# Optimization experiments

Measured on AMD Instinct MI355X. Metric: run time of the kernel, lower is better.

Reference implementation:

```python
import jax, jax.numpy as jnp
import numpy as np


def setup_inputs() -> dict:
    key = jax.random.key(0)
    k1, k2, k3, k4, k5, k6 = jax.random.split(key, 6)
    bs, sl, max_nw, dim_vtw, dim_hidden = 32, 1024, 16, 64, 128
    xw = jax.random.normal(k1, (bs, sl, max_nw, dim_vtw), dtype=jnp.float32)
    # xn: [bs, sl, ns+1]; only last column (word length, in [1, max_nw]) is used
    xn = jax.random.randint(k2, (bs, sl, 4), 1, max_nw + 1)
    s = 1.0 / np.sqrt(dim_hidden)
    W_ih = jax.random.uniform(k3, (4 * dim_hidden, dim_vtw), minval=-s, maxval=s, dtype=jnp.float32)
    W_hh = jax.random.uniform(k4, (4 * dim_hidden, dim_hidden), minval=-s, maxval=s, dtype=jnp.float32)
    b_ih = jax.random.uniform(k5, (4 * dim_hidden,), minval=-s, maxval=s, dtype=jnp.float32)
    b_hh = jax.random.uniform(k6, (4 * dim_hidden,), minval=-s, maxval=s, dtype=jnp.float32)
    return {"xw": xw, "xn": xn, "W_ih": W_ih, "W_hh": W_hh, "b_ih": b_ih, "b_hh": b_hh}


def reference(xw, xn, W_ih, W_hh, b_ih, b_hh):
    # Vectorized equivalent of the original per-group loop: run the LSTM over
    # the full max_nw timesteps for every (b, s) position (LSTM is causal, so
    # the hidden state after nw steps equals running only the first nw steps),
    # then gather h at t = length-1 per position.
    bs, sl, T, D = xw.shape
    H = W_hh.shape[1]
    N = bs * sl
    x = xw.reshape(N, T, D)
    lengths = xn[:, :, -1].reshape(N)
    # Precompute input contributions to all 4 gates: [T, N, 4H]
    x_gates = jnp.einsum('ntd,gd->tng', x, W_ih) + (b_ih + b_hh)

    def step(carry, xg):
        h, c = carry
        gates = xg + h @ W_hh.T  # [N, 4H]
        i, f, g, o = jnp.split(gates, 4, axis=-1)
        i = jax.nn.sigmoid(i)
        f = jax.nn.sigmoid(f)
        g = jnp.tanh(g)
        o = jax.nn.sigmoid(o)
        c = f * c + i * g
        h = o * jnp.tanh(c)
        return (h, c), h

    init = (jnp.zeros((N, H), xw.dtype), jnp.zeros((N, H), xw.dtype))
    _, hs = jax.lax.scan(step, init, x_gates)  # hs: [T, N, H]
    hs = jnp.swapaxes(hs, 0, 1)  # [N, T, H]
    idx = jnp.clip(lengths - 1, 0, T - 1)
    h_final = jnp.take_along_axis(hs, idx[:, None, None], axis=1)[:, 0]  # [N, H]
    return h_final.reshape(bs, sl, H)
```

## Files before the change

kernel.cpp:

```cpp
#include <hip/hip_runtime.h>
#include <math.h>

#define T_STEPS 16
#define DIM_X 64
#define DIM_H 128
#define DIM_K 192
#define NPACK 512
#define MSEQ 64
#define NTHREADS 512
#define LDK 200

typedef __attribute__((ext_vector_type(8))) short bf16x8;
typedef __attribute__((ext_vector_type(4))) float f32x4;

__device__ __forceinline__ float fsigmoid(float x) {
    return 1.0f / (1.0f + __expf(-x));
}
__device__ __forceinline__ float ftanh_(float x) {
    float a = fabsf(x);
    float e = __expf(2.0f * a);
    float r = 1.0f - 2.0f / (e + 1.0f);
    return copysignf(r, x);
}
__device__ __forceinline__ unsigned short bf16_rn(float x) {
    unsigned int b = __float_as_uint(x);
    b += 0x7FFFu + ((b >> 16) & 1u);
    return (unsigned short)(b >> 16);
}
__device__ __forceinline__ float bf16_to_f(unsigned short u) {
    return __uint_as_float(((unsigned int)u) << 16);
}

__global__ void pack_weights(const float* __restrict__ W_ih, const float* __restrict__ W_hh,
                             const float* __restrict__ b_ih, const float* __restrict__ b_hh,
                             unsigned short* __restrict__ Whi, unsigned short* __restrict__ Wlo,
                             float* __restrict__ bsum) {
    int i = blockIdx.x * blockDim.x + threadIdx.x;
    if (i >= NPACK * DIM_K) return;
    int p = i / DIM_K, k = i % DIM_K;
    int g = (p >> 4) & 3;
    int unit = ((p >> 6) << 4) + (p & 15);
    int r = g * DIM_H + unit;
    float v = (k < DIM_X) ? W_ih[r * DIM_X + k] : W_hh[r * DIM_H + (k - DIM_X)];
    unsigned short hi = bf16_rn(v);
    Whi[i] = hi;
    Wlo[i] = bf16_rn(v - bf16_to_f(hi));
    if (k == 0) bsum[p] = b_ih[r] + b_hh[r];
}

__global__ void bin_seqs(const int* __restrict__ xn, int N, int* __restrict__ list) {
    __shared__ int hist[T_STEPS], offs[T_STEPS], cur[T_STEPS];
    int tid = threadIdx.x;
    if (tid < T_STEPS) hist[tid] = 0;
    __syncthreads();
    for (int i = tid; i < N; i += blockDim.x) {
        int len = xn[i * 4 + 3];
        len = min(max(len, 1), T_STEPS);
        atomicAdd(&hist[len - 1], 1);
    }
    __syncthreads();
    if (tid == 0) {
        int acc = 0;
        for (int b = T_STEPS - 1; b >= 0; --b) { offs[b] = acc; acc += hist[b]; }
    }
    __syncthreads();
    if (tid < T_STEPS) cur[tid] = offs[tid];
    __syncthreads();
    for (int i = tid; i < N; i += blockDim.x) {
        int len = xn[i * 4 + 3];
        len = min(max(len, 1), T_STEPS);
        int pos = atomicAdd(&cur[len - 1], 1);
        list[pos] = i;
    }
}

__global__ __launch_bounds__(NTHREADS)
void lstm_main(const float* __restrict__ xw, const int* __restrict__ xn,
               const unsigned short* __restrict__ Whi, const unsigned short* __restrict__ Wlo,
               const float* __restrict__ bsum, const int* __restrict__ list,
               int N, float* __restrict__ out)
{
    __shared__ unsigned short xh_hi[MSEQ][LDK];
    __shared__ unsigned short xh_lo[MSEQ][LDK];
    __shared__ int s_seq[MSEQ];
    __shared__ int s_len[MSEQ];
    __shared__ int s_maxlen;

    const int tid = threadIdx.x;
    const int wv = tid >> 6;
    const int lane = tid & 63;
    const int lr = lane & 15;
    const int lh = lane >> 4;
    const int unit = (wv << 4) + lr;

    if (tid == 0) s_maxlen = 0;
    __syncthreads();
    if (tid < MSEQ) {
        int idx = blockIdx.x * MSEQ + tid;
        int seq = (idx < N) ? list[idx] : -1;
        s_seq[tid] = seq;
        int len = 0;
        if (seq >= 0) { len = xn[seq * 4 + 3]; len = min(max(len, 1), T_STEPS); }
        s_len[tid] = len;
        atomicMax(&s_maxlen, len);
    }
#pragma unroll
    for (int m = 0; m < 4; ++m)
#pragma unroll
        for (int j = 0; j < 4; ++j) {
            int s = (m << 4) + (lh << 2) + j;
            xh_hi[s][DIM_X + unit] = 0;
            xh_lo[s][DIM_X + unit] = 0;
        }
    __syncthreads();
    const int maxlen = s_maxlen;

    float bias[4];
#pragma unroll
    for (int g = 0; g < 4; ++g) bias[g] = bsum[(wv << 6) + (g << 4) + lr];

    int lenv[4][4];
#pragma unroll
    for (int m = 0; m < 4; ++m)
#pragma unroll
        for (int j = 0; j < 4; ++j) lenv[m][j] = s_len[(m << 4) + (lh << 2) + j];

    float c[4][4];
#pragma unroll
    for (int m = 0; m < 4; ++m)
#pragma unroll
        for (int j = 0; j < 4; ++j) c[m][j] = 0.0f;

    const int xsl = tid >> 3;
    const int xko = (tid & 7) << 3;
    const long xseq = (long)max(s_seq[xsl], 0);

    {
        const float* xp = xw + ((size_t)xseq * T_STEPS + 0) * DIM_X + xko;
        float4 a = *(const float4*)xp;
        float4 b = *(const float4*)(xp + 4);
        float xv[8] = {a.x, a.y, a.z, a.w, b.x, b.y, b.z, b.w};
        bf16x8 hv, lv;
#pragma unroll
        for (int e = 0; e < 8; ++e) {
            unsigned short h = bf16_rn(xv[e]);
            hv[e] = (short)h;
            lv[e] = (short)bf16_rn(xv[e] - bf16_to_f(h));
        }
        *(bf16x8*)&xh_hi[xsl][xko] = hv;
        *(bf16x8*)&xh_lo[xsl][xko] = lv;
    }

    const unsigned short* __restrict__ wbase_h = Whi + (size_t)(wv << 6) * DIM_K + (lh << 3);
    const unsigned short* __restrict__ wbase_l = Wlo + (size_t)(wv << 6) * DIM_K + (lh << 3);

    for (int t = 0; t < maxlen; ++t) {
        __syncthreads();

        f32x4 acc[4][4];
#pragma unroll
        for (int m = 0; m < 4; ++m)
#pragma unroll
            for (int g = 0; g < 4; ++g)
                acc[m][g] = (f32x4){bias[g], bias[g], bias[g], bias[g]};

        for (int kc = 0; kc < 6; ++kc) {
            const int kb = kc << 5;
            bf16x8 ahi[4], alo[4];
#pragma unroll
            for (int m = 0; m < 4; ++m) {
                ahi[m] = *(const bf16x8*)&xh_hi[(m << 4) + lr][kb + (lh << 3)];
                alo[m] = *(const bf16x8*)&xh_lo[(m << 4) + lr][kb + (lh << 3)];
            }
            bf16x8 bhi[4], blo[4];
#pragma unroll
            for (int g = 0; g < 4; ++g) {
                const size_t off = (size_t)((g << 4) + lr) * DIM_K + kb;
                bhi[g] = *(const bf16x8*)(wbase_h + off);
                blo[g] = *(const bf16x8*)(wbase_l + off);
            }
#pragma unroll
            for (int m = 0; m < 4; ++m)
#pragma unroll
                for (int g = 0; g < 4; ++g) {
                    acc[m][g] = __builtin_amdgcn_mfma_f32_16x16x32_bf16(ahi[m], bhi[g], acc[m][g], 0, 0, 0);
                    acc[m][g] = __builtin_amdgcn_mfma_f32_16x16x32_bf16(alo[m], bhi[g], acc[m][g], 0, 0, 0);
                    acc[m][g] = __builtin_amdgcn_mfma_f32_16x16x32_bf16(ahi[m], blo[g], acc[m][g], 0, 0, 0);
                }
        }

        const bool do_x = (t + 1 < maxlen);
        float4 xa, xb;
        if (do_x) {
            const float* xp = xw + ((size_t)xseq * T_STEPS + (t + 1)) * DIM_X + xko;
            xa = *(const float4*)xp;
            xb = *(const float4*)(xp + 4);
        }

        __syncthreads();

        if (do_x) {
            float xv[8] = {xa.x, xa.y, xa.z, xa.w, xb.x, xb.y, xb.z, xb.w};
            bf16x8 hv, lv;
#pragma unroll
            for (int e = 0; e < 8; ++e) {
                unsigned short h = bf16_rn(xv[e]);
                hv[e] = (short)h;
                lv[e] = (short)bf16_rn(xv[e] - bf16_to_f(h));
            }
            *(bf16x8*)&xh_hi[xsl][xko] = hv;
            *(bf16x8*)&xh_lo[xsl][xko] = lv;
        }

#pragma unroll
        for (int m = 0; m < 4; ++m)
#pragma unroll
            for (int j = 0; j < 4; ++j) {
                float iv = fsigmoid(acc[m][0][j]);
                float fv = fsigmoid(acc[m][1][j]);
                float gv = ftanh_(acc[m][2][j]);
                float ov = fsigmoid(acc[m][3][j]);
                float cv = fv * c[m][j] + iv * gv;
                c[m][j] = cv;
                float hv = ov * ftanh_(cv);
                int s = (m << 4) + (lh << 2) + j;
                unsigned short hh = bf16_rn(hv);
                xh_hi[s][DIM_X + unit] = hh;
                xh_lo[s][DIM_X + unit] = bf16_rn(hv - bf16_to_f(hh));
                if (t == lenv[m][j] - 1) {
                    int gs = s_seq[s];
                    if (gs >= 0) out[(size_t)gs * DIM_H + unit] = hv;
                }
            }
    }
}

extern "C" void kernel_launch(void* const* d_in, const int* in_sizes, int n_in,
                              void* d_out, int out_size, void* d_ws, size_t ws_size,
                              hipStream_t stream) {
    const float* xw   = (const float*)d_in[0];
    const int*   xn   = (const int*)d_in[1];
    const float* W_ih = (const float*)d_in[2];
    const float* W_hh = (const float*)d_in[3];
    const float* b_ih = (const float*)d_in[4];
    const float* b_hh = (const float*)d_in[5];
    float* out = (float*)d_out;

    const int N = in_sizes[0] / (T_STEPS * DIM_X);

    char* ws = (char*)d_ws;
    unsigned short* Whi = (unsigned short*)ws;
    unsigned short* Wlo = (unsigned short*)(ws + 196608);
    float*          bsum = (float*)(ws + 393216);
    int*            list = (int*)(ws + 395264);

    pack_weights<<<(NPACK * DIM_K + 255) / 256, 256, 0, stream>>>(W_ih, W_hh, b_ih, b_hh, Whi, Wlo, bsum);
    bin_seqs<<<1, 1024, 0, stream>>>(xn, N, list);

    const int nblocks = (N + MSEQ - 1) / MSEQ;
    lstm_main<<<nblocks, NTHREADS, 0, stream>>>(xw, xn, Whi, Wlo, bsum, list, N, out);
}
```

Baseline: 505.1 us.

## Use persistent blocks with atomic chunk queue and fuse prep kernels

Merges weight packing and length binning into one prep kernel, which also resets a work counter. The LSTM kernel becomes persistent: at most 256 blocks repeatedly grab 64-sequence chunks via an atomic counter. Because the list is sorted longest-first, the chunk max length is read from its first entry. Input loads and output stores use nontemporal hints. This aims to balance work across CUs and cut launch overhead, at the cost of less latency hiding from co-resident blocks and a shared-memory reuse race risk.

```diff
diff --git a/kernel.cpp b/kernel.cpp
--- a/kernel.cpp
+++ b/kernel.cpp
@@ -9,6 +9,9 @@
 #define MSEQ 64
 #define NTHREADS 512
 #define LDK 200
+#define PREP_THREADS 256
+#define PACK_ITEMS (NPACK * DIM_K)
+#define PACK_BLOCKS (PACK_ITEMS / PREP_THREADS)
 
 typedef __attribute__((ext_vector_type(8))) short bf16x8;
 typedef __attribute__((ext_vector_type(4))) float f32x4;
@@ -31,29 +34,32 @@
     return __uint_as_float(((unsigned int)u) << 16);
 }
 
-__global__ void pack_weights(const float* __restrict__ W_ih, const float* __restrict__ W_hh,
-                             const float* __restrict__ b_ih, const float* __restrict__ b_hh,
-                             unsigned short* __restrict__ Whi, unsigned short* __restrict__ Wlo,
-                             float* __restrict__ bsum) {
-    int i = blockIdx.x * blockDim.x + threadIdx.x;
-    if (i >= NPACK * DIM_K) return;
-    int p = i / DIM_K, k = i % DIM_K;
-    int g = (p >> 4) & 3;
-    int unit = ((p >> 6) << 4) + (p & 15);
-    int r = g * DIM_H + unit;
-    float v = (k < DIM_X) ? W_ih[r * DIM_X + k] : W_hh[r * DIM_H + (k - DIM_X)];
-    unsigned short hi = bf16_rn(v);
-    Whi[i] = hi;
-    Wlo[i] = bf16_rn(v - bf16_to_f(hi));
-    if (k == 0) bsum[p] = b_ih[r] + b_hh[r];
-}
-
-__global__ void bin_seqs(const int* __restrict__ xn, int N, int* __restrict__ list) {
+__global__ __launch_bounds__(PREP_THREADS)
+void prep(const float* __restrict__ W_ih, const float* __restrict__ W_hh,
+          const float* __restrict__ b_ih, const float* __restrict__ b_hh,
+          const int* __restrict__ xn, int N,
+          unsigned short* __restrict__ Whi, unsigned short* __restrict__ Wlo,
+          float* __restrict__ bsum, int* __restrict__ list, int* __restrict__ ctr) {
+    const int b = blockIdx.x;
+    const int tid = threadIdx.x;
+    if (b < PACK_BLOCKS) {
+        int i = b * PREP_THREADS + tid;
+        int p = i / DIM_K, k = i % DIM_K;
+        int g = (p >> 4) & 3;
+        int unit = ((p >> 6) << 4) + (p & 15);
+        int r = g * DIM_H + unit;
+        float v = (k < DIM_X) ? W_ih[r * DIM_X + k] : W_hh[r * DIM_H + (k - DIM_X)];
+        unsigned short hi = bf16_rn(v);
+        Whi[i] = hi;
+        Wlo[i] = bf16_rn(v - bf16_to_f(hi));
+        if (k == 0) bsum[p] = b_ih[r] + b_hh[r];
+        return;
+    }
     __shared__ int hist[T_STEPS], offs[T_STEPS], cur[T_STEPS];
-    int tid = threadIdx.x;
     if (tid < T_STEPS) hist[tid] = 0;
-    __syncthreads();
-    for (int i = tid; i < N; i += blockDim.x) {
+    if (tid == 0) *ctr = 0;
+    __syncthreads();
+    for (int i = tid; i < N; i += PREP_THREADS) {
         int len = xn[i * 4 + 3];
         len = min(max(len, 1), T_STEPS);
         atomicAdd(&hist[len - 1], 1);
@@ -61,12 +67,12 @@
     __syncthreads();
     if (tid == 0) {
         int acc = 0;
-        for (int b = T_STEPS - 1; b >= 0; --b) { offs[b] = acc; acc += hist[b]; }
+        for (int bb = T_STEPS - 1; bb >= 0; --bb) { offs[bb] = acc; acc += hist[bb]; }
     }
     __syncthreads();
     if (tid < T_STEPS) cur[tid] = offs[tid];
     __syncthreads();
-    for (int i = tid; i < N; i += blockDim.x) {
+    for (int i = tid; i < N; i += PREP_THREADS) {
         int len = xn[i * 4 + 3];
         len = min(max(len, 1), T_STEPS);
         int pos = atomicAdd(&cur[len - 1], 1);
@@ -78,13 +84,13 @@
 void lstm_main(const float* __restrict__ xw, const int* __restrict__ xn,
                const unsigned short* __restrict__ Whi, const unsigned short* __restrict__ Wlo,
                const float* __restrict__ bsum, const int* __restrict__ list,
-               int N, float* __restrict__ out)
+               int N, int* __restrict__ ctr, float* __restrict__ out)
 {
     __shared__ unsigned short xh_hi[MSEQ][LDK];
     __shared__ unsigned short xh_lo[MSEQ][LDK];
     __shared__ int s_seq[MSEQ];
     __shared__ int s_len[MSEQ];
-    __shared__ int s_maxlen;
+    __shared__ int s_chunk;
 
     const int tid = threadIdx.x;
     const int wv = tid >> 6;
@@ -92,115 +98,61 @@
     const int lr = lane & 15;
     const int lh = lane >> 4;
     const int unit = (wv << 4) + lr;
-
-    if (tid == 0) s_maxlen = 0;
-    __syncthreads();
-    if (tid < MSEQ) {
-        int idx = blockIdx.x * MSEQ + tid;
-        int seq = (idx < N) ? list[idx] : -1;
-        s_seq[tid] = seq;
-        int len = 0;
-        if (seq >= 0) { len = xn[seq * 4 + 3]; len = min(max(len, 1), T_STEPS); }
-        s_len[tid] = len;
-        atomicMax(&s_maxlen, len);
-    }
-#pragma unroll
-    for (int m = 0; m < 4; ++m)
-#pragma unroll
-        for (int j = 0; j < 4; ++j) {
-            int s = (m << 4) + (lh << 2) + j;
-            xh_hi[s][DIM_X + unit] = 0;
-            xh_lo[s][DIM_X + unit] = 0;
-        }
-    __syncthreads();
-    const int maxlen = s_maxlen;
+    const int nchunks = (N + MSEQ - 1) / MSEQ;
 
     float bias[4];
 #pragma unroll
     for (int g = 0; g < 4; ++g) bias[g] = bsum[(wv << 6) + (g << 4) + lr];
-
-    int lenv[4][4];
-#pragma unroll
-    for (int m = 0; m < 4; ++m)
-#pragma unroll
-        for (int j = 0; j < 4; ++j) lenv[m][j] = s_len[(m << 4) + (lh << 2) + j];
-
-    float c[4][4];
-#pragma unroll
-    for (int m = 0; m < 4; ++m)
-#pragma unroll
-        for (int j = 0; j < 4; ++j) c[m][j] = 0.0f;
+    const unsigned short* __restrict__ wbase_h = Whi + (size_t)(wv << 6) * DIM_K + (lh << 3);
+    const unsigned short* __restrict__ wbase_l = Wlo + (size_t)(wv << 6) * DIM_K + (lh << 3);
 
     const int xsl = tid >> 3;
     const int xko = (tid & 7) << 3;
-    const long xseq = (long)max(s_seq[xsl], 0);
-
-    {
-        const float* xp = xw + ((size_t)xseq * T_STEPS + 0) * DIM_X + xko;
-        float4 a = *(const float4*)xp;
-        float4 b = *(const float4*)(xp + 4);
-        float xv[8] = {a.x, a.y, a.z, a.w, b.x, b.y, b.z, b.w};
-        bf16x8 hv, lv;
-#pragma unroll
-        for (int e = 0; e < 8; ++e) {
-            unsigned short h = bf16_rn(xv[e]);
-            hv[e] = (short)h;
-            lv[e] = (short)bf16_rn(xv[e] - bf16_to_f(h));
+
+    while (true) {
+        if (tid == 0) s_chunk = atomicAdd(ctr, 1);
+        __syncthreads();
+        const int chunk = s_chunk;
+        if (chunk >= nchunks) break;
+
+        if (tid < MSEQ) {
+            int idx = chunk * MSEQ + tid;
+            int seq = (idx < N) ? list[idx] : -1;
+            s_seq[tid] = seq;
+            int len = 0;
+            if (seq >= 0) { len = xn[seq * 4 + 3]; len = min(max(len, 1), T_STEPS); }
+            s_len[tid] = len;
         }
-        *(bf16x8*)&xh_hi[xsl][xko] = hv;
-        *(bf16x8*)&xh_lo[xsl][xko] = lv;
-    }
-
-    const unsigned short* __restrict__ wbase_h = Whi + (size_t)(wv << 6) * DIM_K + (lh << 3);
-    const unsigned short* __restrict__ wbase_l = Wlo + (size_t)(wv << 6) * DIM_K + (lh << 3);
-
-    for (int t = 0; t < maxlen; ++t) {
+#pragma unroll
+        for (int m = 0; m < 4; ++m)
+#pragma unroll
+            for (int j = 0; j < 4; ++j) {
+                int s = (m << 4) + (lh << 2) + j;
+                xh_hi[s][DIM_X + unit] = 0;
+                xh_lo[s][DIM_X + unit] = 0;
+            }
         __syncthreads();
 
-        f32x4 acc[4][4];
+        const int maxlen = s_len[0];
+        int lenv[4][4];
 #pragma unroll
         for (int m = 0; m < 4; ++m)
 #pragma unroll
-            for (int g = 0; g < 4; ++g)
-                acc[m][g] = (f32x4){bias[g], bias[g], bias[g], bias[g]};
-
-        for (int kc = 0; kc < 6; ++kc) {
-            const int kb = kc << 5;
-            bf16x8 ahi[4], alo[4];
-#pragma unroll
-            for (int m = 0; m < 4; ++m) {
-                ahi[m] = *(const bf16x8*)&xh_hi[(m << 4) + lr][kb + (lh << 3)];
-                alo[m] = *(const bf16x8*)&xh_lo[(m << 4) + lr][kb + (lh << 3)];
-            }
-            bf16x8 bhi[4], blo[4];
-#pragma unroll
-            for (int g = 0; g < 4; ++g) {
-                const size_t off = (size_t)((g << 4) + lr) * DIM_K + kb;
-                bhi[g] = *(const bf16x8*)(wbase_h + off);
-                blo[g] = *(const bf16x8*)(wbase_l + off);
-            }
-#pragma unroll
-            for (int m = 0; m < 4; ++m)
-#pragma unroll
-                for (int g = 0; g < 4; ++g) {
-                    acc[m][g] = __builtin_amdgcn_mfma_f32_16x16x32_bf16(ahi[m], bhi[g], acc[m][g], 0, 0, 0);
-                    acc[m][g] = __builtin_amdgcn_mfma_f32_16x16x32_bf16(alo[m], bhi[g], acc[m][g], 0, 0, 0);
-                    acc[m][g] = __builtin_amdgcn_mfma_f32_16x16x32_bf16(ahi[m], blo[g], acc[m][g], 0, 0, 0);
-                }
-        }
-
-        const bool do_x = (t + 1 < maxlen);
-        float4 xa, xb;
-        if (do_x) {
-            const float* xp = xw + ((size_t)xseq * T_STEPS + (t + 1)) * DIM_X + xko;
-            xa = *(const float4*)xp;
-            xb = *(const float4*)(xp + 4);
-        }
-
-        __syncthreads();
-
-        if (do_x) {
-            float xv[8] = {xa.x, xa.y, xa.z, xa.w, xb.x, xb.y, xb.z, xb.w};
+            for (int j = 0; j < 4; ++j) lenv[m][j] = s_len[(m << 4) + (lh << 2) + j];
+
+        float c[4][4];
+#pragma unroll
+        for (int m = 0; m < 4; ++m)
+#pragma unroll
+            for (int j = 0; j < 4; ++j) c[m][j] = 0.0f;
+
+        const long xseq = (long)max(s_seq[xsl], 0);
+
+        {
+            const float* xp = xw + ((size_t)xseq * T_STEPS + 0) * DIM_X + xko;
+            f32x4 a = __builtin_nontemporal_load((const f32x4*)xp);
+            f32x4 bq = __builtin_nontemporal_load((const f32x4*)(xp + 4));
+            float xv[8] = {a[0], a[1], a[2], a[3], bq[0], bq[1], bq[2], bq[3]};
             bf16x8 hv, lv;
 #pragma unroll
             for (int e = 0; e < 8; ++e) {
@@ -212,26 +164,86 @@
             *(bf16x8*)&xh_lo[xsl][xko] = lv;
         }
 
-#pragma unroll
-        for (int m = 0; m < 4; ++m)
-#pragma unroll
-            for (int j = 0; j < 4; ++j) {
-                float iv = fsigmoid(acc[m][0][j]);
-                float fv = fsigmoid(acc[m][1][j]);
-                float gv = ftanh_(acc[m][2][j]);
-                float ov = fsigmoid(acc[m][3][j]);
-                float cv = fv * c[m][j] + iv * gv;
-                c[m][j] = cv;
-                float hv = ov * ftanh_(cv);
-                int s = (m << 4) + (lh << 2) + j;
-                unsigned short hh = bf16_rn(hv);
-                xh_hi[s][DIM_X + unit] = hh;
-                xh_lo[s][DIM_X + unit] = bf16_rn(hv - bf16_to_f(hh));
-                if (t == lenv[m][j] - 1) {
-                    int gs = s_seq[s];
-                    if (gs >= 0) out[(size_t)gs * DIM_H + unit] = hv;
-                }
-            }
+        for (int t = 0; t < maxlen; ++t) {
+            __syncthreads();
+
+            f32x4 acc[4][4];
+#pragma unroll
+            for (int m = 0; m < 4; ++m)
+#pragma unroll
+                for (int g = 0; g < 4; ++g)
+                    acc[m][g] = (f32x4){bias[g], bias[g], bias[g], bias[g]};
+
+            for (int kc = 0; kc < 6; ++kc) {
+                const int kb = kc << 5;
+                bf16x8 ahi[4], alo[4];
+#pragma unroll
+                for (int m = 0; m < 4; ++m) {
+                    ahi[m] = *(const bf16x8*)&xh_hi[(m << 4) + lr][kb + (lh << 3)];
+                    alo[m] = *(const bf16x8*)&xh_lo[(m << 4) + lr][kb + (lh << 3)];
+                }
+                bf16x8 bhi[4], blo[4];
+#pragma unroll
+                for (int g = 0; g < 4; ++g) {
+                    const size_t off = (size_t)((g << 4) + lr) * DIM_K + kb;
+                    bhi[g] = *(const bf16x8*)(wbase_h + off);
+                    blo[g] = *(const bf16x8*)(wbase_l + off);
+                }
+#pragma unroll
+                for (int m = 0; m < 4; ++m)
+#pragma unroll
+                    for (int g = 0; g < 4; ++g) {
+                        acc[m][g] = __builtin_amdgcn_mfma_f32_16x16x32_bf16(ahi[m], bhi[g], acc[m][g], 0, 0, 0);
+                        acc[m][g] = __builtin_amdgcn_mfma_f32_16x16x32_bf16(alo[m], bhi[g], acc[m][g], 0, 0, 0);
+                        acc[m][g] = __builtin_amdgcn_mfma_f32_16x16x32_bf16(ahi[m], blo[g], acc[m][g], 0, 0, 0);
+                    }
+            }
+
+            const bool do_x = (t + 1 < maxlen);
+            f32x4 xa, xb;
+            if (do_x) {
+                const float* xp = xw + ((size_t)xseq * T_STEPS + (t + 1)) * DIM_X + xko;
+                xa = __builtin_nontemporal_load((const f32x4*)xp);
+                xb = __builtin_nontemporal_load((const f32x4*)(xp + 4));
+            }
+
+            __syncthreads();
+
+            if (do_x) {
+                float xv[8] = {xa[0], xa[1], xa[2], xa[3], xb[0], xb[1], xb[2], xb[3]};
+                bf16x8 hv, lv;
+#pragma unroll
+                for (int e = 0; e < 8; ++e) {
+                    unsigned short h = bf16_rn(xv[e]);
+                    hv[e] = (short)h;
+                    lv[e] = (short)bf16_rn(xv[e] - bf16_to_f(h));
+                }
+                *(bf16x8*)&xh_hi[xsl][xko] = hv;
+                *(bf16x8*)&xh_lo[xsl][xko] = lv;
+            }
+
+#pragma unroll
+            for (int m = 0; m < 4; ++m)
+#pragma unroll
+                for (int j = 0; j < 4; ++j) {
+                    float iv = fsigmoid(acc[m][0][j]);
+                    float fv = fsigmoid(acc[m][1][j]);
+                    float gv = ftanh_(acc[m][2][j]);
+                    float ov = fsigmoid(acc[m][3][j]);
+                    float cv = fv * c[m][j] + iv * gv;
+                    c[m][j] = cv;
+                    float hv = ov * ftanh_(cv);
+                    int s = (m << 4) + (lh << 2) + j;
+                    unsigned short hh = bf16_rn(hv);
+                    xh_hi[s][DIM_X + unit] = hh;
+                    xh_lo[s][DIM_X + unit] = bf16_rn(hv - bf16_to_f(hh));
+                    if (t == lenv[m][j] - 1) {
+                        int gs = s_seq[s];
+                        if (gs >= 0)
+                            __builtin_nontemporal_store(hv, &out[(size_t)gs * DIM_H + unit]);
+                    }
+                }
+        }
     }
 }
 
@@ -249,14 +261,16 @@
     const int N = in_sizes[0] / (T_STEPS * DIM_X);
 
     char* ws = (char*)d_ws;
-    unsigned short* Whi = (unsigned short*)ws;
-    unsigned short* Wlo = (unsigned short*)(ws + 196608);
+    unsigned short* Whi  = (unsigned short*)ws;
+    unsigned short* Wlo  = (unsigned short*)(ws + 196608);
     float*          bsum = (float*)(ws + 393216);
-    int*            list = (int*)(ws + 395264);
-
-    pack_weights<<<(NPACK * DIM_K + 255) / 256, 256, 0, stream>>>(W_ih, W_hh, b_ih, b_hh, Whi, Wlo, bsum);
-    bin_seqs<<<1, 1024, 0, stream>>>(xn, N, list);
-
-    const int nblocks = (N + MSEQ - 1) / MSEQ;
-    lstm_main<<<nblocks, NTHREADS, 0, stream>>>(xw, xn, Whi, Wlo, bsum, list, N, out);
-}
+    int*            ctr  = (int*)(ws + 395264);
+    int*            list = (int*)(ws + 395328);
+
+    prep<<<PACK_BLOCKS + 1, PREP_THREADS, 0, stream>>>(W_ih, W_hh, b_ih, b_hh, xn, N,
+                                                       Whi, Wlo, bsum, list, ctr);
+
+    const int nchunks = (N + MSEQ - 1) / MSEQ;
+    const int nblocks = min(256, nchunks);
+    lstm_main<<<nblocks, NTHREADS, 0, stream>>>(xw, xn, Whi, Wlo, bsum, list, N, ctr, out);
+}
```

Result: slower. 560.2 us (+10.9%).
